# Kernel tuning notes

Hardware: AMD Instinct MI355X
Metric: run time of the kernel (lower is better)

## Reference

```python
import jax, jax.numpy as jnp
import numpy as np

N = 100000      # nodes
E = 600000      # edges
IN, OUT = 128, 32
L1 = IN - (IN - OUT) // 3          # 96
L2 = IN - (2 * (IN - OUT)) // 3    # 64


def setup_inputs() -> dict:
    key = jax.random.key(0)
    ks = jax.random.split(key, 12)

    def lin(k, i, o):
        return jax.random.normal(k, (i, o), jnp.float32) / np.float32(np.sqrt(i))

    return {
        "x": jax.random.normal(ks[0], (N, IN), jnp.float32),
        "edge_index": jax.random.randint(ks[1], (2, E), 0, N, dtype=jnp.int32),
        # ClusterGCNConv 1: lin_out (W,b) + lin_root (no bias)
        "W1": lin(ks[2], IN, L1), "b1": jnp.zeros((L1,), jnp.float32), "Wr1": lin(ks[3], IN, L1),
        # ClusterGCNConv 2
        "W2": lin(ks[4], L1, L2), "b2": jnp.zeros((L2,), jnp.float32), "Wr2": lin(ks[5], L1, L2),
        # GCNConv mu / logstd heads
        "Wmu": lin(ks[6], L2, OUT), "bmu": jnp.zeros((OUT,), jnp.float32),
        "Wls": lin(ks[7], L2, OUT), "bls": jnp.zeros((OUT,), jnp.float32),
    }


def _with_self_loops(edge_index, n):
    loops = jnp.arange(n, dtype=edge_index.dtype)
    src = jnp.concatenate([edge_index[0], loops])
    dst = jnp.concatenate([edge_index[1], loops])
    return src, dst


def _cluster_gcn(x, edge_index, W, b, Wr, n):
    # PyG ClusterGCNConv (diag_lambda=0): out = (D^{-1} (A+I)) x @ W + b + x @ Wr
    src, dst = _with_self_loops(edge_index, n)
    deg = jax.ops.segment_sum(jnp.ones_like(dst, x.dtype), dst, num_segments=n)
    dinv = 1.0 / jnp.clip(deg, 1.0)
    agg = jax.ops.segment_sum(x[src] * dinv[dst][:, None], dst, num_segments=n)
    return agg @ W + b + x @ Wr


def _gcn(x, edge_index, W, b, n):
    # PyG GCNConv: h = x @ W; out = D^{-1/2} (A+I) D^{-1/2} h + b
    h = x @ W
    src, dst = _with_self_loops(edge_index, n)
    deg = jax.ops.segment_sum(jnp.ones_like(dst, h.dtype), dst, num_segments=n)
    dis = jax.lax.rsqrt(jnp.clip(deg, 1.0))  # deg >= 1 thanks to self loops
    norm = dis[src] * dis[dst]
    return jax.ops.segment_sum(h[src] * norm[:, None], dst, num_segments=n) + b


def reference(x, edge_index, W1, b1, Wr1, W2, b2, Wr2, Wmu, bmu, Wls, bls):
    n = x.shape[0]
    h = jax.nn.relu(_cluster_gcn(x, edge_index, W1, b1, Wr1, n))
    h = jax.nn.relu(_cluster_gcn(h, edge_index, W2, b2, Wr2, n))
    return (_gcn(h, edge_index, Wmu, bmu, n), _gcn(h, edge_index, Wls, bls, n))
```

## Files before the change

kernel.cpp:

```cpp
#include <hip/hip_runtime.h>

#define TPB 256
#define GTPB 512

typedef __attribute__((ext_vector_type(8))) short          bf8_t;
typedef __attribute__((ext_vector_type(8))) unsigned short us8_t;
typedef __attribute__((ext_vector_type(4))) float          f4_t;
typedef __attribute__((ext_vector_type(4))) unsigned short us4_t;

__device__ __forceinline__ unsigned short f2bf(float f) {
    union { float f; unsigned u; } v; v.f = f;
    unsigned r = v.u + 0x7FFFu + ((v.u >> 16) & 1u);
    return (unsigned short)(r >> 16);
}
__device__ __forceinline__ float bf2f(unsigned short u) {
    union { unsigned u; float f; } v; v.u = (unsigned)u << 16; return v.f;
}


__global__ void k_count(const int* __restrict__ ei, int E, int* __restrict__ cnt) {
    int e = blockIdx.x * TPB + threadIdx.x;
    if (e < E) atomicAdd(&cnt[ei[E + e]], 1);
}

__global__ void k_blocksum(const int* __restrict__ cnt, int n, int* __restrict__ bsum) {
    __shared__ int s[TPB];
    int t = threadIdx.x, i = blockIdx.x * TPB + t;
    s[t] = (i < n) ? cnt[i] : 0;
    __syncthreads();
    for (int off = TPB / 2; off > 0; off >>= 1) {
        if (t < off) s[t] += s[t + off];
        __syncthreads();
    }
    if (t == 0) bsum[blockIdx.x] = s[0];
}

__global__ void k_scan_bsum(int* __restrict__ bsum, int nb) {
    __shared__ int s[512];
    int t = threadIdx.x;
    int v = (t < nb) ? bsum[t] : 0;
    s[t] = v; __syncthreads();
    for (int off = 1; off < 512; off <<= 1) {
        int x = (t >= off) ? s[t - off] : 0;
        __syncthreads();
        s[t] += x;
        __syncthreads();
    }
    if (t < nb) bsum[t] = s[t] - v;
}

__global__ void k_rowptr(const int* __restrict__ cnt, const int* __restrict__ bsum, int n, int E,
                         int* __restrict__ rowptr, int* __restrict__ cursor,
                         float* __restrict__ dinv, float* __restrict__ dis) {
    __shared__ int s[TPB];
    int t = threadIdx.x, i = blockIdx.x * TPB + t;
    int v = (i < n) ? cnt[i] : 0;
    s[t] = v; __syncthreads();
    for (int off = 1; off < TPB; off <<= 1) {
        int x = (t >= off) ? s[t - off] : 0;
        __syncthreads();
        s[t] += x;
        __syncthreads();
    }
    if (i < n) {
        int start = bsum[blockIdx.x] + s[t] - v;
        rowptr[i] = start;
        cursor[i] = start;
        float d = (float)(v + 1);
        dinv[i] = 1.0f / d;
        dis[i]  = rsqrtf(d);
    }
    if (i == 0) rowptr[n] = E;
}

__global__ void k_fill(const int* __restrict__ ei, int E,
                       int* __restrict__ cursor, int* __restrict__ col) {
    int e = blockIdx.x * TPB + threadIdx.x;
    if (e < E) {
        int src = ei[e], dst = ei[E + e];
        int p = atomicAdd(&cursor[dst], 1);
        col[p] = src;
    }
}

__global__ void k_wconv(const float* W1, const float* Wr1, const float* W2, const float* Wr2,
                        const float* Wmu, const float* Wls,
                        unsigned short* T1, unsigned short* Tr1, unsigned short* T2,
                        unsigned short* Tr2, unsigned short* Tmu, unsigned short* Tls) {
    const float* W; unsigned short* T; int K, M;
    switch (blockIdx.y) {
        case 0: W = W1;  T = T1;  K = 128; M = 96; break;
        case 1: W = Wr1; T = Tr1; K = 128; M = 96; break;
        case 2: W = W2;  T = T2;  K = 96;  M = 64; break;
        case 3: W = Wr2; T = Tr2; K = 96;  M = 64; break;
        case 4: W = Wmu; T = Tmu; K = 64;  M = 32; break;
        default:W = Wls; T = Tls; K = 64;  M = 32; break;
    }
    int idx = blockIdx.x * TPB + threadIdx.x;
    if (idx < K * M) {
        int m = idx / K, k = idx % K;
        T[idx] = f2bf(W[k * M + m]);
    }
}

template <int K, int M, bool AF32>
__global__ __launch_bounds__(GTPB, 6) void k_gemm5(const void* __restrict__ Av,
                                                   const unsigned short* __restrict__ WT,
                                                   unsigned short* __restrict__ Y,
                                                   unsigned short* __restrict__ R,
                                                   int n, int nt) {
    constexpr int KS = K / 32;
    constexpr int ST = K + 8;
    constexpr int MF = M / 2;
    __shared__ unsigned short Bs[M * ST];
    for (int i = threadIdx.x * 8; i < M * K; i += GTPB * 8) {
        int m = i / K, k = i - m * K;
        *(us8_t*)(Bs + m * ST + k) = *(const us8_t*)(WT + i);
    }
    __syncthreads();

    int lane = threadIdx.x & 63;
    int wave = threadIdx.x >> 6;
    int quad = lane >> 4;
    int l15  = lane & 15;

    for (int tile = blockIdx.x; tile < nt; tile += gridDim.x) {
        int base = tile * 128 + wave * 16;
        int rA = base + l15; if (rA > n - 1) rA = n - 1;

        bf8_t a[KS];
        if (AF32) {
            const float* ap = (const float*)Av + (size_t)rA * K + quad * 8;
#pragma unroll
            for (int s = 0; s < KS; s++) {
                f4_t lo = *(const f4_t*)(ap + s * 32);
                f4_t hi = *(const f4_t*)(ap + s * 32 + 4);
                bf8_t t;
                t[0] = (short)f2bf(lo.x); t[1] = (short)f2bf(lo.y);
                t[2] = (short)f2bf(lo.z); t[3] = (short)f2bf(lo.w);
                t[4] = (short)f2bf(hi.x); t[5] = (short)f2bf(hi.y);
                t[6] = (short)f2bf(hi.z); t[7] = (short)f2bf(hi.w);
                a[s] = t;
            }
        } else {
            const unsigned short* ap = (const unsigned short*)Av + (size_t)rA * K + quad * 8;
#pragma unroll
            for (int s = 0; s < KS; s++) a[s] = *(const bf8_t*)(ap + s * 32);
        }

        int row = base + quad * 4;
#pragma unroll 3
        for (int ct = 0; ct < M / 16; ct++) {
            const unsigned short* bp = Bs + (ct * 16 + l15) * ST + quad * 8;
            f4_t acc = {0.f, 0.f, 0.f, 0.f};
#pragma unroll
            for (int s = 0; s < KS; s++) {
                bf8_t b = *(const bf8_t*)(bp + s * 32);
                acc = __builtin_amdgcn_mfma_f32_16x16x32_bf16(a[s], b, acc, 0, 0, 0);
            }
            int colg = ct * 16 + l15;
            unsigned short* dst = (colg < MF) ? (Y + colg) : (R + (colg - MF));
#pragma unroll
            for (int r = 0; r < 4; r++) {
                if (row + r < n) dst[(size_t)(row + r) * MF] = f2bf(acc[r]);
            }
        }
    }
}

__global__ __launch_bounds__(GTPB, 6) void k_gemm_out5(const unsigned short* __restrict__ Z,
                                                       const unsigned short* __restrict__ WT,
                                                       const float* __restrict__ bmu,
                                                       const float* __restrict__ bls,
                                                       float* __restrict__ out, int n, int nt) {
    constexpr int K = 64, M = 64, KS = 2, ST = K + 8;
    __shared__ unsigned short Bs[M * ST];
    for (int i = threadIdx.x * 8; i < M * K; i += GTPB * 8) {
        int m = i / K, k = i - m * K;
        *(us8_t*)(Bs + m * ST + k) = *(const us8_t*)(WT + i);
    }
    __syncthreads();

    int lane = threadIdx.x & 63;
    int wave = threadIdx.x >> 6;
    int quad = lane >> 4;
    int l15  = lane & 15;

    for (int tile = blockIdx.x; tile < nt; tile += gridDim.x) {
        int base = tile * 128 + wave * 16;
        int rA = base + l15; if (rA > n - 1) rA = n - 1;
        const unsigned short* ap = Z + (size_t)rA * K + quad * 8;
        bf8_t a[KS];
#pragma unroll
        for (int s = 0; s < KS; s++) a[s] = *(const bf8_t*)(ap + s * 32);

        int row = base + quad * 4;
#pragma unroll 2
        for (int ct = 0; ct < M / 16; ct++) {
            const unsigned short* bp = Bs + (ct * 16 + l15) * ST + quad * 8;
            f4_t acc = {0.f, 0.f, 0.f, 0.f};
#pragma unroll
            for (int s = 0; s < KS; s++) {
                bf8_t b = *(const bf8_t*)(bp + s * 32);
                acc = __builtin_amdgcn_mfma_f32_16x16x32_bf16(a[s], b, acc, 0, 0, 0);
            }
            int colg = ct * 16 + l15;
            float bias = (colg < 32) ? bmu[colg] : bls[colg - 32];
            float* dst = (colg < 32) ? (out + colg) : (out + (size_t)n * 32 + (colg - 32));
#pragma unroll
            for (int r = 0; r < 4; r++) {
                if (row + r < n) dst[(size_t)(row + r) * 32] = acc[r] + bias;
            }
        }
    }
}

template <int MF, int GRP, bool SCALE>
__global__ __launch_bounds__(TPB) void k_aggc(const unsigned short* __restrict__ Y,
                                              const unsigned short* __restrict__ R,
                                              const float* __restrict__ bias,
                                              const float* __restrict__ dinv,
                                              const float* __restrict__ dis,
                                              const int* __restrict__ rowptr,
                                              const int* __restrict__ col,
                                              unsigned short* __restrict__ Hb, int n) {
    int idx = blockIdx.x * TPB + threadIdx.x;
    int g = idx / GRP;
    int l = idx - g * GRP;
    if (g >= n) return;
    int c = l * 8;
    int r0 = rowptr[g], r1 = rowptr[g + 1];
    float acc[8];
    {
        bf8_t v = *(const bf8_t*)(Y + (size_t)g * MF + c);
#pragma unroll
        for (int j = 0; j < 8; j++) acc[j] = bf2f((unsigned short)v[j]);
    }
    int e = r0;
    for (; e + 4 <= r1; e += 4) {
        int s0 = col[e], s1 = col[e + 1], s2 = col[e + 2], s3 = col[e + 3];
        bf8_t v0 = *(const bf8_t*)(Y + (size_t)s0 * MF + c);
        bf8_t v1 = *(const bf8_t*)(Y + (size_t)s1 * MF + c);
        bf8_t v2 = *(const bf8_t*)(Y + (size_t)s2 * MF + c);
        bf8_t v3 = *(const bf8_t*)(Y + (size_t)s3 * MF + c);
#pragma unroll
        for (int j = 0; j < 8; j++)
            acc[j] += (bf2f((unsigned short)v0[j]) + bf2f((unsigned short)v1[j]))
                    + (bf2f((unsigned short)v2[j]) + bf2f((unsigned short)v3[j]));
    }
    for (; e < r1; ++e) {
        int s = col[e];
        bf8_t v = *(const bf8_t*)(Y + (size_t)s * MF + c);
#pragma unroll
        for (int j = 0; j < 8; j++) acc[j] += bf2f((unsigned short)v[j]);
    }
    float di = dinv[g];
    float sc = SCALE ? dis[g] : 1.0f;
    bf8_t rr = *(const bf8_t*)(R + (size_t)g * MF + c);
    us8_t o;
#pragma unroll
    for (int j = 0; j < 8; j++) {
        float h = fmaxf(acc[j] * di + bf2f((unsigned short)rr[j]) + bias[c + j], 0.f);
        o[j] = f2bf(SCALE ? sc * h : h);
    }
    *(us8_t*)(Hb + (size_t)g * MF + c) = o;
}

__global__ __launch_bounds__(TPB) void k_agghead(const unsigned short* __restrict__ H2s,
                                                 const float* __restrict__ dis,
                                                 const int* __restrict__ rowptr,
                                                 const int* __restrict__ col,
                                                 unsigned short* __restrict__ Z, int n) {
    const int GRP = 8;
    int g = blockIdx.x * (TPB / GRP) + threadIdx.x / GRP;
    int l = threadIdx.x & (GRP - 1);
    if (g >= n) return;
    int c = l * 8;
    int r0 = rowptr[g], r1 = rowptr[g + 1];
    float acc[8];
    {
        bf8_t v = *(const bf8_t*)(H2s + (size_t)g * 64 + c);
#pragma unroll
        for (int j = 0; j < 8; j++) acc[j] = bf2f((unsigned short)v[j]);
    }
    int e = r0;
    for (; e + 4 <= r1; e += 4) {
        int s0 = col[e], s1 = col[e + 1], s2 = col[e + 2], s3 = col[e + 3];
        bf8_t v0 = *(const bf8_t*)(H2s + (size_t)s0 * 64 + c);
        bf8_t v1 = *(const bf8_t*)(H2s + (size_t)s1 * 64 + c);
        bf8_t v2 = *(const bf8_t*)(H2s + (size_t)s2 * 64 + c);
        bf8_t v3 = *(const bf8_t*)(H2s + (size_t)s3 * 64 + c);
#pragma unroll
        for (int j = 0; j < 8; j++)
            acc[j] += (bf2f((unsigned short)v0[j]) + bf2f((unsigned short)v1[j]))
                    + (bf2f((unsigned short)v2[j]) + bf2f((unsigned short)v3[j]));
    }
    for (; e < r1; ++e) {
        int s = col[e];
        bf8_t v = *(const bf8_t*)(H2s + (size_t)s * 64 + c);
#pragma unroll
        for (int j = 0; j < 8; j++) acc[j] += bf2f((unsigned short)v[j]);
    }
    float dg = dis[g];
    us8_t o;
#pragma unroll
    for (int j = 0; j < 8; j++) o[j] = f2bf(dg * acc[j]);
    *(us8_t*)(Z + (size_t)g * 64 + c) = o;
}


extern "C" void kernel_launch(void* const* d_in, const int* in_sizes, int n_in,
                              void* d_out, int out_size, void* d_ws, size_t ws_size,
                              hipStream_t stream) {
    const float* x   = (const float*)d_in[0];
    const int*   ei  = (const int*)d_in[1];
    const float* W1  = (const float*)d_in[2];
    const float* b1  = (const float*)d_in[3];
    const float* Wr1 = (const float*)d_in[4];
    const float* W2  = (const float*)d_in[5];
    const float* b2  = (const float*)d_in[6];
    const float* Wr2 = (const float*)d_in[7];
    const float* Wmu = (const float*)d_in[8];
    const float* bmu = (const float*)d_in[9];
    const float* Wls = (const float*)d_in[10];
    const float* bls = (const float*)d_in[11];
    float* out = (float*)d_out;

    const int IN = 128, L1F = 96, L2F = 64;
    const int N = in_sizes[0] / IN;
    const int E = in_sizes[1] / 2;

    char* ws = (char*)d_ws;
    size_t off = 0;
    auto alloc = [&](size_t b) { size_t r = off; off += (b + 255) & ~(size_t)255; return r; };

    const int nb = (N + TPB - 1) / TPB;
    int*   cnt  = (int*)(ws + alloc((size_t)N * 4));
    int*   bsum = (int*)(ws + alloc((size_t)nb * 4));
    int*   rowp = (int*)(ws + alloc((size_t)(N + 1) * 4));
    int*   curs = (int*)(ws + alloc((size_t)N * 4));
    int*   col  = (int*)(ws + alloc((size_t)E * 4));
    float* dinv = (float*)(ws + alloc((size_t)N * 4));
    float* dis  = (float*)(ws + alloc((size_t)N * 4));
    unsigned short* T1  = (unsigned short*)(ws + alloc((size_t)IN  * L1F * 2));
    unsigned short* Tr1 = (unsigned short*)(ws + alloc((size_t)IN  * L1F * 2));
    unsigned short* T2  = (unsigned short*)(ws + alloc((size_t)L1F * L2F * 2));
    unsigned short* Tr2 = (unsigned short*)(ws + alloc((size_t)L1F * L2F * 2));
    unsigned short* Tmu = (unsigned short*)(ws + alloc((size_t)L2F * 32 * 2));
    unsigned short* Tls = (unsigned short*)(ws + alloc((size_t)L2F * 32 * 2));
    unsigned short* Y1  = (unsigned short*)(ws + alloc((size_t)N * L1F * 2));
    unsigned short* R1  = (unsigned short*)(ws + alloc((size_t)N * L1F * 2));
    unsigned short* Y2  = (unsigned short*)(ws + alloc((size_t)N * L2F * 2));
    unsigned short* R2  = (unsigned short*)(ws + alloc((size_t)N * L2F * 2));
    unsigned short* Hb1 = (unsigned short*)(ws + alloc((size_t)N * L1F * 2));
    unsigned short* H2s = (unsigned short*)(ws + alloc((size_t)N * L2F * 2));
    unsigned short* Zag = (unsigned short*)(ws + alloc((size_t)N * L2F * 2));

    hipMemsetAsync(cnt, 0, (size_t)N * 4, stream);

    dim3 eg((E + TPB - 1) / TPB);
    k_count<<<eg, TPB, 0, stream>>>(ei, E, cnt);
    k_blocksum<<<nb, TPB, 0, stream>>>(cnt, N, bsum);
    k_scan_bsum<<<1, 512, 0, stream>>>(bsum, nb);
    k_rowptr<<<nb, TPB, 0, stream>>>(cnt, bsum, N, E, rowp, curs, dinv, dis);
    k_fill<<<eg, TPB, 0, stream>>>(ei, E, curs, col);

    k_wconv<<<dim3(48, 6), TPB, 0, stream>>>(W1, Wr1, W2, Wr2, Wmu, Wls,
                                             T1, Tr1, T2, Tr2, Tmu, Tls);

    const int nt = (N + 127) / 128;
    k_gemm5<128, 192, true><<<nt, GTPB, 0, stream>>>(x, T1, Y1, R1, N, nt);
    k_aggc<96, 12, false><<<((size_t)N * 12 + TPB - 1) / TPB, TPB, 0, stream>>>(
        Y1, R1, b1, dinv, dis, rowp, col, Hb1, N);

    k_gemm5<96, 128, false><<<nt, GTPB, 0, stream>>>(Hb1, T2, Y2, R2, N, nt);
    k_aggc<64, 8, true><<<((size_t)N * 8 + TPB - 1) / TPB, TPB, 0, stream>>>(
        Y2, R2, b2, dinv, dis, rowp, col, H2s, N);

    k_agghead<<<(N + 31) / 32, TPB, 0, stream>>>(H2s, dis, rowp, col, Zag, N);
    k_gemm_out5<<<nt, GTPB, 0, stream>>>(Zag, Tmu, bmu, bls, out, N, nt);
}
```

Before: 321.3 us.

## Aggregate before GEMM and fuse root path into concatenated-K GEMM

Reorders each ClusterGCN layer to aggregate raw features first (gather over X, scaled by dinv) and then run one GEMM over the concatenated [agg | x] input with stacked [W; Wr] weights. Bias, ReLU and the optional dis scaling move into the GEMM epilogue. x is converted to bf16 once up front. In layer 1 this means gathering 128-wide rows instead of 96-wide projections and writing a P1 intermediate, in exchange for dropping the separate Y/R outputs and the fused aggregation epilogue.

```diff
diff --git a/kernel.cpp b/kernel.cpp
--- a/kernel.cpp
+++ b/kernel.cpp
@@ -83,147 +83,45 @@
     }
 }
 
+
+__global__ void k_xconv(const float* __restrict__ x, unsigned short* __restrict__ xb, long total4) {
+    long i = (long)blockIdx.x * TPB + threadIdx.x;
+    if (i < total4) {
+        f4_t v = *(const f4_t*)(x + i * 4);
+        us4_t o;
+        o.x = f2bf(v.x); o.y = f2bf(v.y); o.z = f2bf(v.z); o.w = f2bf(v.w);
+        *(us4_t*)(xb + i * 4) = o;
+    }
+}
+
 __global__ void k_wconv(const float* W1, const float* Wr1, const float* W2, const float* Wr2,
                         const float* Wmu, const float* Wls,
-                        unsigned short* T1, unsigned short* Tr1, unsigned short* T2,
-                        unsigned short* Tr2, unsigned short* Tmu, unsigned short* Tls) {
-    const float* W; unsigned short* T; int K, M;
-    switch (blockIdx.y) {
-        case 0: W = W1;  T = T1;  K = 128; M = 96; break;
-        case 1: W = Wr1; T = Tr1; K = 128; M = 96; break;
-        case 2: W = W2;  T = T2;  K = 96;  M = 64; break;
-        case 3: W = Wr2; T = Tr2; K = 96;  M = 64; break;
-        case 4: W = Wmu; T = Tmu; K = 64;  M = 32; break;
-        default:W = Wls; T = Tls; K = 64;  M = 32; break;
-    }
+                        unsigned short* T1c, unsigned short* T2c, unsigned short* THc) {
     int idx = blockIdx.x * TPB + threadIdx.x;
-    if (idx < K * M) {
-        int m = idx / K, k = idx % K;
-        T[idx] = f2bf(W[k * M + m]);
-    }
-}
-
-template <int K, int M, bool AF32>
-__global__ __launch_bounds__(GTPB, 6) void k_gemm5(const void* __restrict__ Av,
-                                                   const unsigned short* __restrict__ WT,
-                                                   unsigned short* __restrict__ Y,
-                                                   unsigned short* __restrict__ R,
-                                                   int n, int nt) {
-    constexpr int KS = K / 32;
-    constexpr int ST = K + 8;
-    constexpr int MF = M / 2;
-    __shared__ unsigned short Bs[M * ST];
-    for (int i = threadIdx.x * 8; i < M * K; i += GTPB * 8) {
-        int m = i / K, k = i - m * K;
-        *(us8_t*)(Bs + m * ST + k) = *(const us8_t*)(WT + i);
-    }
-    __syncthreads();
-
-    int lane = threadIdx.x & 63;
-    int wave = threadIdx.x >> 6;
-    int quad = lane >> 4;
-    int l15  = lane & 15;
-
-    for (int tile = blockIdx.x; tile < nt; tile += gridDim.x) {
-        int base = tile * 128 + wave * 16;
-        int rA = base + l15; if (rA > n - 1) rA = n - 1;
-
-        bf8_t a[KS];
-        if (AF32) {
-            const float* ap = (const float*)Av + (size_t)rA * K + quad * 8;
-#pragma unroll
-            for (int s = 0; s < KS; s++) {
-                f4_t lo = *(const f4_t*)(ap + s * 32);
-                f4_t hi = *(const f4_t*)(ap + s * 32 + 4);
-                bf8_t t;
-                t[0] = (short)f2bf(lo.x); t[1] = (short)f2bf(lo.y);
-                t[2] = (short)f2bf(lo.z); t[3] = (short)f2bf(lo.w);
-                t[4] = (short)f2bf(hi.x); t[5] = (short)f2bf(hi.y);
-                t[6] = (short)f2bf(hi.z); t[7] = (short)f2bf(hi.w);
-                a[s] = t;
-            }
-        } else {
-            const unsigned short* ap = (const unsigned short*)Av + (size_t)rA * K + quad * 8;
-#pragma unroll
-            for (int s = 0; s < KS; s++) a[s] = *(const bf8_t*)(ap + s * 32);
-        }
-
-        int row = base + quad * 4;
-#pragma unroll 3
-        for (int ct = 0; ct < M / 16; ct++) {
-            const unsigned short* bp = Bs + (ct * 16 + l15) * ST + quad * 8;
-            f4_t acc = {0.f, 0.f, 0.f, 0.f};
-#pragma unroll
-            for (int s = 0; s < KS; s++) {
-                bf8_t b = *(const bf8_t*)(bp + s * 32);
-                acc = __builtin_amdgcn_mfma_f32_16x16x32_bf16(a[s], b, acc, 0, 0, 0);
-            }
-            int colg = ct * 16 + l15;
-            unsigned short* dst = (colg < MF) ? (Y + colg) : (R + (colg - MF));
-#pragma unroll
-            for (int r = 0; r < 4; r++) {
-                if (row + r < n) dst[(size_t)(row + r) * MF] = f2bf(acc[r]);
-            }
-        }
-    }
-}
-
-__global__ __launch_bounds__(GTPB, 6) void k_gemm_out5(const unsigned short* __restrict__ Z,
-                                                       const unsigned short* __restrict__ WT,
-                                                       const float* __restrict__ bmu,
-                                                       const float* __restrict__ bls,
-                                                       float* __restrict__ out, int n, int nt) {
-    constexpr int K = 64, M = 64, KS = 2, ST = K + 8;
-    __shared__ unsigned short Bs[M * ST];
-    for (int i = threadIdx.x * 8; i < M * K; i += GTPB * 8) {
-        int m = i / K, k = i - m * K;
-        *(us8_t*)(Bs + m * ST + k) = *(const us8_t*)(WT + i);
-    }
-    __syncthreads();
-
-    int lane = threadIdx.x & 63;
-    int wave = threadIdx.x >> 6;
-    int quad = lane >> 4;
-    int l15  = lane & 15;
-
-    for (int tile = blockIdx.x; tile < nt; tile += gridDim.x) {
-        int base = tile * 128 + wave * 16;
-        int rA = base + l15; if (rA > n - 1) rA = n - 1;
-        const unsigned short* ap = Z + (size_t)rA * K + quad * 8;
-        bf8_t a[KS];
-#pragma unroll
-        for (int s = 0; s < KS; s++) a[s] = *(const bf8_t*)(ap + s * 32);
-
-        int row = base + quad * 4;
-#pragma unroll 2
-        for (int ct = 0; ct < M / 16; ct++) {
-            const unsigned short* bp = Bs + (ct * 16 + l15) * ST + quad * 8;
-            f4_t acc = {0.f, 0.f, 0.f, 0.f};
-#pragma unroll
-            for (int s = 0; s < KS; s++) {
-                bf8_t b = *(const bf8_t*)(bp + s * 32);
-                acc = __builtin_amdgcn_mfma_f32_16x16x32_bf16(a[s], b, acc, 0, 0, 0);
-            }
-            int colg = ct * 16 + l15;
-            float bias = (colg < 32) ? bmu[colg] : bls[colg - 32];
-            float* dst = (colg < 32) ? (out + colg) : (out + (size_t)n * 32 + (colg - 32));
-#pragma unroll
-            for (int r = 0; r < 4; r++) {
-                if (row + r < n) dst[(size_t)(row + r) * 32] = acc[r] + bias;
-            }
-        }
-    }
-}
-
-template <int MF, int GRP, bool SCALE>
-__global__ __launch_bounds__(TPB) void k_aggc(const unsigned short* __restrict__ Y,
-                                              const unsigned short* __restrict__ R,
-                                              const float* __restrict__ bias,
-                                              const float* __restrict__ dinv,
-                                              const float* __restrict__ dis,
-                                              const int* __restrict__ rowptr,
-                                              const int* __restrict__ col,
-                                              unsigned short* __restrict__ Hb, int n) {
+    if (blockIdx.y == 0) {
+        if (idx < 96 * 256) {
+            int m = idx / 256, k = idx % 256;
+            T1c[idx] = f2bf(k < 128 ? W1[k * 96 + m] : Wr1[(k - 128) * 96 + m]);
+        }
+    } else if (blockIdx.y == 1) {
+        if (idx < 64 * 192) {
+            int m = idx / 192, k = idx % 192;
+            T2c[idx] = f2bf(k < 96 ? W2[k * 64 + m] : Wr2[(k - 96) * 64 + m]);
+        }
+    } else {
+        if (idx < 64 * 64) {
+            int m = idx / 64, k = idx % 64;
+            THc[idx] = f2bf(m < 32 ? Wmu[k * 32 + m] : Wls[k * 32 + (m - 32)]);
+        }
+    }
+}
+
+template <int MF, int GRP>
+__global__ __launch_bounds__(TPB) void k_aggpre(const unsigned short* __restrict__ X,
+                                                const float* __restrict__ sc,
+                                                const int* __restrict__ rowptr,
+                                                const int* __restrict__ col,
+                                                unsigned short* __restrict__ P, int n) {
     int idx = blockIdx.x * TPB + threadIdx.x;
     int g = idx / GRP;
     int l = idx - g * GRP;
@@ -232,17 +130,17 @@
     int r0 = rowptr[g], r1 = rowptr[g + 1];
     float acc[8];
     {
-        bf8_t v = *(const bf8_t*)(Y + (size_t)g * MF + c);
+        bf8_t v = *(const bf8_t*)(X + (size_t)g * MF + c);
 #pragma unroll
         for (int j = 0; j < 8; j++) acc[j] = bf2f((unsigned short)v[j]);
     }
     int e = r0;
     for (; e + 4 <= r1; e += 4) {
         int s0 = col[e], s1 = col[e + 1], s2 = col[e + 2], s3 = col[e + 3];
-        bf8_t v0 = *(const bf8_t*)(Y + (size_t)s0 * MF + c);
-        bf8_t v1 = *(const bf8_t*)(Y + (size_t)s1 * MF + c);
-        bf8_t v2 = *(const bf8_t*)(Y + (size_t)s2 * MF + c);
-        bf8_t v3 = *(const bf8_t*)(Y + (size_t)s3 * MF + c);
+        bf8_t v0 = *(const bf8_t*)(X + (size_t)s0 * MF + c);
+        bf8_t v1 = *(const bf8_t*)(X + (size_t)s1 * MF + c);
+        bf8_t v2 = *(const bf8_t*)(X + (size_t)s2 * MF + c);
+        bf8_t v3 = *(const bf8_t*)(X + (size_t)s3 * MF + c);
 #pragma unroll
         for (int j = 0; j < 8; j++)
             acc[j] += (bf2f((unsigned short)v0[j]) + bf2f((unsigned short)v1[j]))
@@ -250,62 +148,121 @@
     }
     for (; e < r1; ++e) {
         int s = col[e];
-        bf8_t v = *(const bf8_t*)(Y + (size_t)s * MF + c);
+        bf8_t v = *(const bf8_t*)(X + (size_t)s * MF + c);
 #pragma unroll
         for (int j = 0; j < 8; j++) acc[j] += bf2f((unsigned short)v[j]);
     }
-    float di = dinv[g];
-    float sc = SCALE ? dis[g] : 1.0f;
-    bf8_t rr = *(const bf8_t*)(R + (size_t)g * MF + c);
+    float s = sc[g];
     us8_t o;
 #pragma unroll
-    for (int j = 0; j < 8; j++) {
-        float h = fmaxf(acc[j] * di + bf2f((unsigned short)rr[j]) + bias[c + j], 0.f);
-        o[j] = f2bf(SCALE ? sc * h : h);
-    }
-    *(us8_t*)(Hb + (size_t)g * MF + c) = o;
-}
-
-__global__ __launch_bounds__(TPB) void k_agghead(const unsigned short* __restrict__ H2s,
-                                                 const float* __restrict__ dis,
-                                                 const int* __restrict__ rowptr,
-                                                 const int* __restrict__ col,
-                                                 unsigned short* __restrict__ Z, int n) {
-    const int GRP = 8;
-    int g = blockIdx.x * (TPB / GRP) + threadIdx.x / GRP;
-    int l = threadIdx.x & (GRP - 1);
-    if (g >= n) return;
-    int c = l * 8;
-    int r0 = rowptr[g], r1 = rowptr[g + 1];
-    float acc[8];
-    {
-        bf8_t v = *(const bf8_t*)(H2s + (size_t)g * 64 + c);
-#pragma unroll
-        for (int j = 0; j < 8; j++) acc[j] = bf2f((unsigned short)v[j]);
-    }
-    int e = r0;
-    for (; e + 4 <= r1; e += 4) {
-        int s0 = col[e], s1 = col[e + 1], s2 = col[e + 2], s3 = col[e + 3];
-        bf8_t v0 = *(const bf8_t*)(H2s + (size_t)s0 * 64 + c);
-        bf8_t v1 = *(const bf8_t*)(H2s + (size_t)s1 * 64 + c);
-        bf8_t v2 = *(const bf8_t*)(H2s + (size_t)s2 * 64 + c);
-        bf8_t v3 = *(const bf8_t*)(H2s + (size_t)s3 * 64 + c);
-#pragma unroll
-        for (int j = 0; j < 8; j++)
-            acc[j] += (bf2f((unsigned short)v0[j]) + bf2f((unsigned short)v1[j]))
-                    + (bf2f((unsigned short)v2[j]) + bf2f((unsigned short)v3[j]));
-    }
-    for (; e < r1; ++e) {
-        int s = col[e];
-        bf8_t v = *(const bf8_t*)(H2s + (size_t)s * 64 + c);
-#pragma unroll
-        for (int j = 0; j < 8; j++) acc[j] += bf2f((unsigned short)v[j]);
-    }
-    float dg = dis[g];
-    us8_t o;
-#pragma unroll
-    for (int j = 0; j < 8; j++) o[j] = f2bf(dg * acc[j]);
-    *(us8_t*)(Z + (size_t)g * 64 + c) = o;
+    for (int j = 0; j < 8; j++) o[j] = f2bf(s * acc[j]);
+    *(us8_t*)(P + (size_t)g * MF + c) = o;
+}
+
+template <int K, int M, int EPI>
+__global__ __launch_bounds__(GTPB, 6) void k_gemm8(const unsigned short* __restrict__ A1,
+                                                   const unsigned short* __restrict__ A2,
+                                                   const unsigned short* __restrict__ WT,
+                                                   const float* __restrict__ bias,
+                                                   const float* __restrict__ dis,
+                                                   unsigned short* __restrict__ O,
+                                                   int n, int nt) {
+    constexpr int KS = K / 32;
+    constexpr int KH = K / 2;
+    constexpr int ST = K + 8;
+    __shared__ unsigned short Bs[M * ST];
+    for (int i = threadIdx.x * 8; i < M * K; i += GTPB * 8) {
+        int m = i / K, k = i - m * K;
+        *(us8_t*)(Bs + m * ST + k) = *(const us8_t*)(WT + i);
+    }
+    __syncthreads();
+
+    int lane = threadIdx.x & 63;
+    int wave = threadIdx.x >> 6;
+    int quad = lane >> 4;
+    int l15  = lane & 15;
+
+    for (int tile = blockIdx.x; tile < nt; tile += gridDim.x) {
+        int base = tile * 128 + wave * 16;
+        int rA = base + l15; if (rA > n - 1) rA = n - 1;
+
+        bf8_t a[KS];
+        {
+            const unsigned short* p1 = A1 + (size_t)rA * KH + quad * 8;
+            const unsigned short* p2 = A2 + (size_t)rA * KH + quad * 8;
+#pragma unroll
+            for (int s = 0; s < KS / 2; s++) a[s] = *(const bf8_t*)(p1 + s * 32);
+#pragma unroll
+            for (int s = 0; s < KS / 2; s++) a[KS / 2 + s] = *(const bf8_t*)(p2 + s * 32);
+        }
+
+        int row0 = base + quad * 4;
+#pragma unroll 3
+        for (int ct = 0; ct < M / 16; ct++) {
+            const unsigned short* bp = Bs + (ct * 16 + l15) * ST + quad * 8;
+            f4_t acc = {0.f, 0.f, 0.f, 0.f};
+#pragma unroll
+            for (int s = 0; s < KS; s++) {
+                bf8_t b = *(const bf8_t*)(bp + s * 32);
+                acc = __builtin_amdgcn_mfma_f32_16x16x32_bf16(a[s], b, acc, 0, 0, 0);
+            }
+            int colg = ct * 16 + l15;
+            float bb = bias[colg];
+#pragma unroll
+            for (int r = 0; r < 4; r++) {
+                int row = row0 + r;
+                if (row < n) {
+                    float h = fmaxf(acc[r] + bb, 0.f);
+                    if (EPI == 1) h *= dis[row];
+                    O[(size_t)row * M + colg] = f2bf(h);
+                }
+            }
+        }
+    }
+}
+
+__global__ __launch_bounds__(GTPB, 6) void k_gemm8h(const unsigned short* __restrict__ Z,
+                                                    const unsigned short* __restrict__ WT,
+                                                    const float* __restrict__ bmu,
+                                                    const float* __restrict__ bls,
+                                                    float* __restrict__ out, int n, int nt) {
+    constexpr int K = 64, M = 64, KS = 2, ST = K + 8;
+    __shared__ unsigned short Bs[M * ST];
+    for (int i = threadIdx.x * 8; i < M * K; i += GTPB * 8) {
+        int m = i / K, k = i - m * K;
+        *(us8_t*)(Bs + m * ST + k) = *(const us8_t*)(WT + i);
+    }
+    __syncthreads();
+
+    int lane = threadIdx.x & 63;
+    int wave = threadIdx.x >> 6;
+    int quad = lane >> 4;
+    int l15  = lane & 15;
+
+    for (int tile = blockIdx.x; tile < nt; tile += gridDim.x) {
+        int base = tile * 128 + wave * 16;
+        int rA = base + l15; if (rA > n - 1) rA = n - 1;
+        const unsigned short* ap = Z + (size_t)rA * K + quad * 8;
+        bf8_t a0 = *(const bf8_t*)(ap);
+        bf8_t a1 = *(const bf8_t*)(ap + 32);
+
+        int row0 = base + quad * 4;
+#pragma unroll
+        for (int ct = 0; ct < M / 16; ct++) {
+            const unsigned short* bp = Bs + (ct * 16 + l15) * ST + quad * 8;
+            f4_t acc = {0.f, 0.f, 0.f, 0.f};
+            acc = __builtin_amdgcn_mfma_f32_16x16x32_bf16(a0, *(const bf8_t*)bp, acc, 0, 0, 0);
+            acc = __builtin_amdgcn_mfma_f32_16x16x32_bf16(a1, *(const bf8_t*)(bp + 32), acc, 0, 0, 0);
+            int colg = ct * 16 + l15;
+            float bb = (colg < 32) ? bmu[colg] : bls[colg - 32];
+            float* dst = (colg < 32) ? (out + colg) : (out + (size_t)n * 32 + (colg - 32));
+#pragma unroll
+            for (int r = 0; r < 4; r++) {
+                int row = row0 + r;
+                if (row < n) dst[(size_t)row * 32] = acc[r] + bb;
+            }
+        }
+    }
 }
 
 
@@ -342,17 +299,13 @@
     int*   col  = (int*)(ws + alloc((size_t)E * 4));
     float* dinv = (float*)(ws + alloc((size_t)N * 4));
     float* dis  = (float*)(ws + alloc((size_t)N * 4));
-    unsigned short* T1  = (unsigned short*)(ws + alloc((size_t)IN  * L1F * 2));
-    unsigned short* Tr1 = (unsigned short*)(ws + alloc((size_t)IN  * L1F * 2));
-    unsigned short* T2  = (unsigned short*)(ws + alloc((size_t)L1F * L2F * 2));
-    unsigned short* Tr2 = (unsigned short*)(ws + alloc((size_t)L1F * L2F * 2));
-    unsigned short* Tmu = (unsigned short*)(ws + alloc((size_t)L2F * 32 * 2));
-    unsigned short* Tls = (unsigned short*)(ws + alloc((size_t)L2F * 32 * 2));
-    unsigned short* Y1  = (unsigned short*)(ws + alloc((size_t)N * L1F * 2));
-    unsigned short* R1  = (unsigned short*)(ws + alloc((size_t)N * L1F * 2));
-    unsigned short* Y2  = (unsigned short*)(ws + alloc((size_t)N * L2F * 2));
-    unsigned short* R2  = (unsigned short*)(ws + alloc((size_t)N * L2F * 2));
+    unsigned short* T1c = (unsigned short*)(ws + alloc((size_t)96 * 256 * 2));
+    unsigned short* T2c = (unsigned short*)(ws + alloc((size_t)64 * 192 * 2));
+    unsigned short* THc = (unsigned short*)(ws + alloc((size_t)64 * 64 * 2));
+    unsigned short* Xb  = (unsigned short*)(ws + alloc((size_t)N * IN * 2));
+    unsigned short* P1  = (unsigned short*)(ws + alloc((size_t)N * IN * 2));
     unsigned short* Hb1 = (unsigned short*)(ws + alloc((size_t)N * L1F * 2));
+    unsigned short* P2  = (unsigned short*)(ws + alloc((size_t)N * L1F * 2));
     unsigned short* H2s = (unsigned short*)(ws + alloc((size_t)N * L2F * 2));
     unsigned short* Zag = (unsigned short*)(ws + alloc((size_t)N * L2F * 2));
 
@@ -365,18 +318,17 @@
     k_rowptr<<<nb, TPB, 0, stream>>>(cnt, bsum, N, E, rowp, curs, dinv, dis);
     k_fill<<<eg, TPB, 0, stream>>>(ei, E, curs, col);
 
-    k_wconv<<<dim3(48, 6), TPB, 0, stream>>>(W1, Wr1, W2, Wr2, Wmu, Wls,
-                                             T1, Tr1, T2, Tr2, Tmu, Tls);
+    long x4 = (long)N * IN / 4;
+    k_xconv<<<(unsigned)((x4 + TPB - 1) / TPB), TPB, 0, stream>>>(x, Xb, x4);
+    k_wconv<<<dim3(96, 3), TPB, 0, stream>>>(W1, Wr1, W2, Wr2, Wmu, Wls, T1c, T2c, THc);
 
     const int nt = (N + 127) / 128;
-    k_gemm5<128, 192, true><<<nt, GTPB, 0, stream>>>(x, T1, Y1, R1, N, nt);
-    k_aggc<96, 12, false><<<((size_t)N * 12 + TPB - 1) / TPB, TPB, 0, stream>>>(
-        Y1, R1, b1, dinv, dis, rowp, col, Hb1, N);
-
-    k_gemm5<96, 128, false><<<nt, GTPB, 0, stream>>>(Hb1, T2, Y2, R2, N, nt);
-    k_aggc<64, 8, true><<<((size_t)N * 8 + TPB - 1) / TPB, TPB, 0, stream>>>(
-        Y2, R2, b2, dinv, dis, rowp, col, H2s, N);
-
-    k_agghead<<<(N + 31) / 32, TPB, 0, stream>>>(H2s, dis, rowp, col, Zag, N);
-    k_gemm_out5<<<nt, GTPB, 0, stream>>>(Zag, Tmu, bmu, bls, out, N, nt);
-}
+    k_aggpre<128, 16><<<((size_t)N * 16 + TPB - 1) / TPB, TPB, 0, stream>>>(Xb, dinv, rowp, col, P1, N);
+    k_gemm8<256, 96, 0><<<nt, GTPB, 0, stream>>>(P1, Xb, T1c, b1, nullptr, Hb1, N, nt);
+
+    k_aggpre<96, 12><<<((size_t)N * 12 + TPB - 1) / TPB, TPB, 0, stream>>>(Hb1, dinv, rowp, col, P2, N);
+    k_gemm8<192, 64, 1><<<nt, GTPB, 0, stream>>>(P2, Hb1, T2c, b2, dis, H2s, N, nt);
+
+    k_aggpre<64, 8><<<((size_t)N * 8 + TPB - 1) / TPB, TPB, 0, stream>>>(H2s, dis, rowp, col, Zag, N);
+    k_gemm8h<<<nt, GTPB, 0, stream>>>(Zag, THc, bmu, bls, out, N, nt);
+}
```

After: 355.6 us. 10.7% more time.
